# Kernel tuning notes

Measured on AMD Instinct MI355X. Metric: run time of the kernel, lower is better.

Reference implementation:

```python
import jax, jax.numpy as jnp
import numpy as np

REG = 1e-6

def maxpool2(x):  # NCHW, kernel 2 stride 2
    return jax.lax.reduce_window(x, -jnp.inf, jax.lax.max, (1, 1, 2, 2), (1, 1, 2, 2), 'VALID')

def conv2d_same(x, w, b):  # NCHW / OIHW, stride 1, padding 1 (3x3)
    y = jax.lax.conv_general_dilated(x, w, (1, 1), ((1, 1), (1, 1)),
                                     dimension_numbers=('NCHW', 'OIHW', 'NCHW'))
    return y + b[None, :, None, None]

def batch_skew(a):  # [B,3] -> [B,3,3]
    z = jnp.zeros_like(a[:, 0])
    return jnp.stack([
        jnp.stack([z, -a[:, 2], a[:, 1]], -1),
        jnp.stack([a[:, 2], z, -a[:, 0]], -1),
        jnp.stack([-a[:, 1], a[:, 0], z], -1)], 1)

def batch_twist2mat(w):  # Rodrigues: so(3) -> SO(3)
    theta = jnp.maximum(jnp.linalg.norm(w, axis=1, keepdims=True), 1e-12)  # [B,1]
    A = batch_skew(w / theta)
    s = jnp.sin(theta)[:, :, None]
    c = (1.0 - jnp.cos(theta))[:, :, None]
    return jnp.eye(3, dtype=w.dtype) + s * A + c * (A @ A)

def setup_inputs() -> dict:
    key = jax.random.key(0)
    ks = jax.random.split(key, 24)
    B, C, H, W = 64, 8, 240, 320
    HW = H * W
    A = jax.random.normal(ks[0], (B, 6, 6), jnp.float32)
    JtJ = A @ jnp.swapaxes(A, 1, 2) + 6.0 * jnp.eye(6, dtype=jnp.float32)  # SPD Hessian
    inp = {
        'JtJ': JtJ,
        'Jt': jax.random.normal(ks[1], (B, 6, HW), jnp.float32),
        'weights': jax.random.uniform(ks[2], (B, 1, H, W), jnp.float32),
        'R': jax.random.normal(ks[3], (B, 1, H, W), jnp.float32),
        'pose_R': jax.random.normal(ks[4], (B, 3, 3), jnp.float32),
        'pose_t': jax.random.normal(ks[5], (B, 3, 1), jnp.float32),
        'invD0': jax.random.uniform(ks[6], (B, 1, H, W), jnp.float32),
        'invD1': jax.random.uniform(ks[7], (B, 1, H, W), jnp.float32),
        'x0': jax.random.normal(ks[8], (B, C, H, W), jnp.float32),
        'x1': jax.random.normal(ks[9], (B, C, H, W), jnp.float32),
        'K': jax.random.normal(ks[10], (B, 3, 3), jnp.float32),
        # DampingNet parameters
        'consts': jax.random.normal(ks[11], (6, 6), jnp.float32),
        'conv1_w': jax.random.normal(ks[12], (8, 1, 3, 3), jnp.float32) * 0.2,
        'conv1_b': jnp.zeros((8,), jnp.float32),
        'conv2_w': jax.random.normal(ks[13], (16, 8, 3, 3), jnp.float32) * 0.1,
        'conv2_b': jnp.zeros((16,), jnp.float32),
        'fc1_w': jax.random.normal(ks[14], (64, 19200), jnp.float32) * 0.01,
        'fc1_b': jnp.zeros((64,), jnp.float32),
        'fc2_w': jax.random.normal(ks[15], (6, 64), jnp.float32) * 0.1,
        'fc2_b': jnp.zeros((6,), jnp.float32),
    }
    return inp

def dampingnet(R, consts, c1w, c1b, c2w, c2b, f1w, f1b, f2w, f2b):
    B = R.shape[0]
    h = maxpool2(R)
    h = jax.nn.relu(conv2d_same(h, c1w, c1b))
    h = maxpool2(h)
    h = jax.nn.relu(conv2d_same(h, c2w, c2b))
    h = maxpool2(h)
    h = h.reshape(B, -1)  # [B, 19200], NCHW flatten matches torch
    h = jax.nn.relu(h @ f1w.T + f1b)
    lambdas_w = jax.nn.softmax(h @ f2w.T + f2b, axis=-1)  # [B,6]
    wc = lambdas_w @ consts  # [B,6]
    min_, max_ = -6.0, -5.0
    return 10.0 ** (min_ + jax.nn.sigmoid(wc) * (max_ - min_))  # [B,6]

def reference(JtJ, Jt, weights, R, pose_R, pose_t, invD0, invD1, x0, x1, K,
              consts, conv1_w, conv1_b, conv2_w, conv2_b, fc1_w, fc1_b, fc2_w, fc2_b):
    B = JtJ.shape[0]
    wR = (weights * R).reshape(B, -1, 1)            # [B,HW,1]
    JtR = Jt @ wR                                   # [B,6,1]
    lam = dampingnet(R, consts, conv1_w, conv1_b, conv2_w, conv2_b,
                     fc1_w, fc1_b, fc2_w, fc2_b)    # [B,6]
    trace = jnp.trace(JtJ, axis1=1, axis2=2)        # [B]
    diag_add = lam + 1e-6 * trace[:, None]          # [B,6]
    eye6 = jnp.eye(6, dtype=JtJ.dtype)
    Hessian = JtJ + diag_add[:, :, None] * eye6     # diag_mask*lambda + epsilon
    # inverse_update_pose: regularized batched 6x6 inverse
    Hinv = jnp.linalg.inv(Hessian + REG * eye6)
    xi = Hinv @ JtR                                 # [B,6,1]
    d_R = batch_twist2mat(-xi[:, :3, 0])            # [B,3,3]
    d_t = -(d_R @ xi[:, 3:])                        # [B,3,1]
    R_new = pose_R @ d_R
    t_new = pose_R @ d_t + pose_t
    return jnp.concatenate([R_new, t_new], axis=2)  # [B,3,4] pose (R|t)
```

## Files before the change

kernel.cpp:

```cpp
#include <hip/hip_runtime.h>
#include <math.h>

#define BATCH 64
#define WW 320
#define HWTOT 76800
#define HW4 19200
#define NJTRB 512
#define JSL4 2400
#define NCONV1 1280
#define KS 64
#define NSLICE 300

typedef _Float16 half2_t __attribute__((ext_vector_type(2)));
union U32H2 { unsigned int u; half2_t h; };
__device__ __forceinline__ unsigned int pack_h2(float a, float b) {
  U32H2 x; x.h = half2_t{(_Float16)a, (_Float16)b}; return x.u;
}
__device__ __forceinline__ half2_t u_as_h2(unsigned int u) { U32H2 x; x.u = u; return x.h; }

#if defined(__has_builtin)
#if __has_builtin(__builtin_amdgcn_fdot2)
#define HAVE_FDOT2 1
#endif
#endif

__device__ __forceinline__ float dot2acc(unsigned int a, unsigned int b, float c) {
#ifdef HAVE_FDOT2
  return __builtin_amdgcn_fdot2(u_as_h2(a), u_as_h2(b), c, false);
#else
  half2_t ah = u_as_h2(a), bh = u_as_h2(b);
  return c + (float)ah.x * (float)bh.x + (float)ah.y * (float)bh.y;
#endif
}

__global__ __launch_bounds__(256) void k_front(
    const float* __restrict__ Jt, const float* __restrict__ wgt,
    const float* __restrict__ Rin, const float* __restrict__ c1w,
    const float* __restrict__ c1b, const float* __restrict__ c2w,
    float* __restrict__ part, unsigned int* __restrict__ h1u,
    unsigned int* __restrict__ wpk) {
  __shared__ float smem[34 * 37 + 96];
  int tid = threadIdx.x;
  if (blockIdx.x < NJTRB) {
    int b = blockIdx.x >> 3, s = blockIdx.x & 7;
    const float4* w4 = (const float4*)(wgt + (size_t)b * HWTOT);
    const float4* r4 = (const float4*)(Rin + (size_t)b * HWTOT);
    const float4* j4 = (const float4*)(Jt + (size_t)b * 6 * HWTOT);
    int base = s * JSL4;
    float acc[6] = {0.f, 0.f, 0.f, 0.f, 0.f, 0.f};
#pragma unroll 3
    for (int k = 0; k < 9; ++k) {
      int t = base + k * 256 + tid;
      float4 wv = w4[t], rv = r4[t];
      float4 p;
      p.x = wv.x * rv.x; p.y = wv.y * rv.y; p.z = wv.z * rv.z; p.w = wv.w * rv.w;
#pragma unroll
      for (int i = 0; i < 6; ++i) {
        float4 jv = j4[i * HW4 + t];
        acc[i] += jv.x * p.x + jv.y * p.y + jv.z * p.z + jv.w * p.w;
      }
    }
    if (tid < 96) {
      int t = base + 2304 + tid;
      float4 wv = w4[t], rv = r4[t];
      float4 p;
      p.x = wv.x * rv.x; p.y = wv.y * rv.y; p.z = wv.z * rv.z; p.w = wv.w * rv.w;
#pragma unroll
      for (int i = 0; i < 6; ++i) {
        float4 jv = j4[i * HW4 + t];
        acc[i] += jv.x * p.x + jv.y * p.y + jv.z * p.z + jv.w * p.w;
      }
    }
#pragma unroll
    for (int i = 0; i < 6; ++i) {
      float v = acc[i];
      for (int off = 32; off; off >>= 1) v += __shfl_down(v, off, 64);
      acc[i] = v;
    }
    float* sred = smem;
    int lane = tid & 63, wid = tid >> 6;
    if (lane == 0) {
#pragma unroll
      for (int i = 0; i < 6; ++i) sred[wid * 6 + i] = acc[i];
    }
    __syncthreads();
    if (tid < 6) {
      part[blockIdx.x * 6 + tid] =
          sred[0 + tid] + sred[6 + tid] + sred[12 + tid] + sred[18 + tid];
    }
    return;
  }
  int cb = blockIdx.x - NJTRB;
  int b = cb / 20, rem = cb % 20;
  int by = rem / 5, bx = rem % 5;
  if (cb == 0) {
    for (int i = tid; i < 576; i += 256) {
      int ocg = i / 288, tap = (i % 288) / 32, o = (i % 32) / 4, icp = i % 4;
      int oc = ocg * 8 + o;
      float lo = c2w[oc * 72 + (2 * icp) * 9 + tap];
      float hi = c2w[oc * 72 + (2 * icp + 1) * 9 + tap];
      wpk[i] = pack_h2(lo, hi);
    }
  }
  float (*sA)[37] = (float(*)[37])smem;
  float* sW = smem + 34 * 37;
  float* sB = sW + 72;
  if (tid < 72) sW[tid] = c1w[(tid & 7) * 9 + (tid >> 3)];
  if (tid < 8) sB[tid] = c1b[tid];
  int iy0 = 32 * by - 1;
  const float* src = Rin + (size_t)b * HWTOT;
  for (int idx = tid; idx < 34 * 18; idx += 256) {
    int pr = idx / 18, c4 = idx % 18;
    int py = iy0 + pr;
    int gx = 64 * bx - 4 + 4 * c4;
    float cell0 = 0.f, cell1 = 0.f;
    if (py >= 0 && py < 120 && gx >= 0 && gx < 320) {
      const float4* row0 = (const float4*)(src + (size_t)(2 * py) * WW + gx);
      const float4* row1 = (const float4*)(src + (size_t)(2 * py + 1) * WW + gx);
      float4 v0 = row0[0], v1 = row1[0];
      cell0 = fmaxf(fmaxf(v0.x, v0.y), fmaxf(v1.x, v1.y));
      cell1 = fmaxf(fmaxf(v0.z, v0.w), fmaxf(v1.z, v1.w));
    }
    sA[pr][2 * c4] = cell0;
    sA[pr][2 * c4 + 1] = cell1;
  }
  __syncthreads();
  int ly = tid / 16, lx = tid % 16;
  int y = 16 * by + ly, x = 16 * bx + lx;
  float win[16];
#pragma unroll
  for (int r = 0; r < 4; ++r)
#pragma unroll
    for (int c = 0; c < 4; ++c) win[r * 4 + c] = sA[2 * ly + r][2 * lx + c + 1];
  float acc[8][4];
#pragma unroll
  for (int oc = 0; oc < 8; ++oc)
#pragma unroll
    for (int p = 0; p < 4; ++p) acc[oc][p] = 0.f;
#pragma unroll
  for (int tap = 0; tap < 9; ++tap) {
    int ky = tap / 3, kx = tap % 3;
#pragma unroll
    for (int oc = 0; oc < 8; ++oc) {
      float wv = sW[tap * 8 + oc];
#pragma unroll
      for (int py = 0; py < 2; ++py)
#pragma unroll
        for (int px = 0; px < 2; ++px)
          acc[oc][py * 2 + px] += wv * win[(py + ky) * 4 + (px + kx)];
    }
  }
  if (y < 60) {
    float v[8];
#pragma unroll
    for (int oc = 0; oc < 8; ++oc)
      v[oc] = fmaxf(fmaxf(fmaxf(acc[oc][0], acc[oc][1]), fmaxf(acc[oc][2], acc[oc][3])) + sB[oc], 0.f);
    uint4 st;
    st.x = pack_h2(v[0], v[1]);
    st.y = pack_h2(v[2], v[3]);
    st.z = pack_h2(v[4], v[5]);
    st.w = pack_h2(v[6], v[7]);
    *(uint4*)(h1u + (((size_t)b * 60 + y) * 80 + x) * 4) = st;
  }
}

__global__ __launch_bounds__(256) void k_conv2(
    const unsigned int* __restrict__ h1u, const unsigned int* __restrict__ wpk,
    const float* __restrict__ c2b, float* __restrict__ h2) {
  __shared__ __align__(16) uint4 sA[34][36];
  int b = blockIdx.z >> 1, ocg = blockIdx.z & 1;
  int ty0 = blockIdx.y * 16, tx0 = blockIdx.x * 16;
  int tid = threadIdx.x;
  int iy0 = ty0 * 2 - 1, ix0 = tx0 * 2 - 1;
  const unsigned int* src = h1u + (size_t)b * 60 * 80 * 4;
  for (int idx = tid; idx < 34 * 34; idx += 256) {
    int r = idx / 34, c = idx % 34;
    int gy = iy0 + r, gx = ix0 + c;
    uint4 v = make_uint4(0u, 0u, 0u, 0u);
    if (gy >= 0 && gy < 60 && gx >= 0 && gx < 80)
      v = *(const uint4*)(src + ((size_t)gy * 80 + gx) * 4);
    sA[r][c] = v;
  }
  __syncthreads();
  int ly = tid / 16, lx = tid % 16;
  uint4 win[16];
#pragma unroll
  for (int r = 0; r < 4; ++r)
#pragma unroll
    for (int c = 0; c < 4; ++c) win[r * 4 + c] = sA[2 * ly + r][2 * lx + c];
  float acc[8][4];
#pragma unroll
  for (int o = 0; o < 8; ++o)
#pragma unroll
    for (int p = 0; p < 4; ++p) acc[o][p] = 0.f;
  const uint4* wq = (const uint4*)wpk + ocg * 72;
#pragma unroll
  for (int tap = 0; tap < 9; ++tap) {
    int ky = tap / 3, kx = tap % 3;
#pragma unroll
    for (int o = 0; o < 8; ++o) {
      uint4 wv = wq[tap * 8 + o];
#pragma unroll
      for (int py = 0; py < 2; ++py)
#pragma unroll
        for (int px = 0; px < 2; ++px) {
          uint4 wn = win[(py + ky) * 4 + (px + kx)];
          float a = acc[o][py * 2 + px];
          a = dot2acc(wn.x, wv.x, a);
          a = dot2acc(wn.y, wv.y, a);
          a = dot2acc(wn.z, wv.z, a);
          a = dot2acc(wn.w, wv.w, a);
          acc[o][py * 2 + px] = a;
        }
    }
  }
  int y = ty0 + ly, x = tx0 + lx;
  if (y < 30 && x < 40) {
#pragma unroll
    for (int o = 0; o < 8; ++o) {
      int oc = ocg * 8 + o;
      float m = fmaxf(fmaxf(acc[o][0], acc[o][1]), fmaxf(acc[o][2], acc[o][3])) + c2b[oc];
      h2[(((size_t)b * 16 + oc) * 30 + y) * 40 + x] = fmaxf(m, 0.f);
    }
  }
}

__global__ __launch_bounds__(256) void k_fc1_part(
    const float* __restrict__ h2, const float* __restrict__ f1w,
    float* __restrict__ fcpart) {
  __shared__ __align__(16) float sH[KS * 68];
  __shared__ __align__(16) float sWt[KS * 68];
  int sl = blockIdx.x, k0 = sl * KS;
  int tid = threadIdx.x;
  for (int idx = tid; idx < 64 * KS; idx += 256) {
    int b = idx >> 6, kk = idx & 63;
    sH[kk * 68 + b] = h2[(size_t)b * 19200 + k0 + kk];
    sWt[kk * 68 + b] = f1w[(size_t)b * 19200 + k0 + kk];
  }
  __syncthreads();
  int bq = tid & 15, jq = tid >> 4;
  int b0 = bq * 4, j0 = jq * 4;
  float acc[4][4];
#pragma unroll
  for (int i = 0; i < 4; ++i)
#pragma unroll
    for (int j = 0; j < 4; ++j) acc[i][j] = 0.f;
  for (int kk = 0; kk < KS; ++kk) {
    float4 hv = *(const float4*)&sH[kk * 68 + b0];
    float4 wv = *(const float4*)&sWt[kk * 68 + j0];
    float hb[4] = {hv.x, hv.y, hv.z, hv.w};
    float wb[4] = {wv.x, wv.y, wv.z, wv.w};
#pragma unroll
    for (int i = 0; i < 4; ++i)
#pragma unroll
      for (int j = 0; j < 4; ++j) acc[i][j] += hb[i] * wb[j];
  }
#pragma unroll
  for (int i = 0; i < 4; ++i)
#pragma unroll
    for (int j = 0; j < 4; ++j)
      fcpart[(size_t)(b0 + i) * 19200 + sl * 64 + (j0 + j)] = acc[i][j];
}

__global__ __launch_bounds__(256) void k_final(
    const float* __restrict__ fcpart, const float* __restrict__ f1b,
    const float* __restrict__ f2w, const float* __restrict__ f2b,
    const float* __restrict__ consts, const float* __restrict__ part,
    const float* __restrict__ JtJ, const float* __restrict__ poseR,
    const float* __restrict__ poseT, float* __restrict__ out) {
  __shared__ __align__(16) float sred[16 * 64];
  __shared__ float fc1v[64];
  __shared__ float sf2w[384];
  __shared__ float sf2b[8];
  __shared__ float sconst[36];
  __shared__ float lg[6];
  __shared__ float lamv[6];
  __shared__ float jtrv[6];
  int b = blockIdx.x, tid = threadIdx.x;
  for (int i = tid; i < 384; i += 256) sf2w[i] = f2w[i];
  if (tid < 6) sf2b[tid] = f2b[tid];
  if (tid < 36) sconst[tid] = consts[tid];
  {
    const float4* fp4 = (const float4*)(fcpart + (size_t)b * 19200);
    int sg = tid >> 4, j4 = tid & 15;
    float4 a = make_float4(0.f, 0.f, 0.f, 0.f);
    for (int s = sg; s < NSLICE; s += 16) {
      float4 v = fp4[s * 16 + j4];
      a.x += v.x; a.y += v.y; a.z += v.z; a.w += v.w;
    }
    ((float4*)sred)[sg * 16 + j4] = a;
  }
  if (tid >= 64 && tid < 70) {
    int i = tid - 64;
    float v = 0.f;
    for (int s = 0; s < 8; ++s) v += part[(b * 8 + s) * 6 + i];
    jtrv[i] = v;
  }
  __syncthreads();
  if (tid < 64) {
    float v = 0.f;
#pragma unroll
    for (int sg = 0; sg < 16; ++sg) v += sred[sg * 64 + tid];
    fc1v[tid] = fmaxf(v + f1b[tid], 0.f);
  }
  __syncthreads();
  if (tid < 6) {
    float v = sf2b[tid];
#pragma unroll
    for (int k = 0; k < 64; ++k) v += fc1v[k] * sf2w[tid * 64 + k];
    lg[tid] = v;
  }
  __syncthreads();
  if (tid < 6) {
    float m = lg[0];
#pragma unroll
    for (int i = 1; i < 6; ++i) m = fmaxf(m, lg[i]);
    float e[6], ssum = 0.f;
#pragma unroll
    for (int i = 0; i < 6; ++i) { e[i] = expf(lg[i] - m); ssum += e[i]; }
    float inv = 1.f / ssum;
    float wc = 0.f;
#pragma unroll
    for (int i = 0; i < 6; ++i) wc += (e[i] * inv) * sconst[i * 6 + tid];
    float sg = 1.f / (1.f + expf(-wc));
    lamv[tid] = expf((-6.f + sg) * 2.302585092994046f);
  }
  __syncthreads();
  if (tid == 0) {
    float Hm[6][6];
    const float* srcH = JtJ + b * 36;
    float tr = 0.f;
#pragma unroll
    for (int i = 0; i < 6; ++i) {
#pragma unroll
      for (int jj = 0; jj < 6; ++jj) Hm[i][jj] = srcH[i * 6 + jj];
      tr += srcH[i * 6 + i];
    }
    float rhs[6];
#pragma unroll
    for (int i = 0; i < 6; ++i) {
      rhs[i] = jtrv[i];
      Hm[i][i] += lamv[i] + 1e-6f * tr + 1e-6f;
    }
    float L[6][6];
#pragma unroll
    for (int i = 0; i < 6; ++i) {
#pragma unroll
      for (int jj = 0; jj < 6; ++jj) {
        if (jj > i) continue;
        float s = Hm[i][jj];
#pragma unroll
        for (int k = 0; k < 6; ++k)
          if (k < jj) s -= L[i][k] * L[jj][k];
        if (i == jj) L[i][jj] = sqrtf(fmaxf(s, 1e-30f));
        else L[i][jj] = s / L[jj][jj];
      }
    }
    float yv[6];
#pragma unroll
    for (int i = 0; i < 6; ++i) {
      float s = rhs[i];
#pragma unroll
      for (int k = 0; k < 6; ++k)
        if (k < i) s -= L[i][k] * yv[k];
      yv[i] = s / L[i][i];
    }
    float xi[6];
#pragma unroll
    for (int ii = 5; ii >= 0; --ii) {
      float s = yv[ii];
#pragma unroll
      for (int k = 0; k < 6; ++k)
        if (k > ii) s -= L[k][ii] * xi[k];
      xi[ii] = s / L[ii][ii];
    }
    float wx = -xi[0], wy = -xi[1], wz = -xi[2];
    float th = fmaxf(sqrtf(wx * wx + wy * wy + wz * wz), 1e-12f);
    float ux = wx / th, uy = wy / th, uz = wz / th;
    float s = sinf(th), c1 = 1.f - cosf(th);
    float Rd[3][3];
    Rd[0][0] = 1.f + c1 * (ux * ux - 1.f);
    Rd[0][1] = -s * uz + c1 * (ux * uy);
    Rd[0][2] = s * uy + c1 * (ux * uz);
    Rd[1][0] = s * uz + c1 * (uy * ux);
    Rd[1][1] = 1.f + c1 * (uy * uy - 1.f);
    Rd[1][2] = -s * ux + c1 * (uy * uz);
    Rd[2][0] = -s * uy + c1 * (uz * ux);
    Rd[2][1] = s * ux + c1 * (uz * uy);
    Rd[2][2] = 1.f + c1 * (uz * uz - 1.f);
    float dt[3];
#pragma unroll
    for (int r = 0; r < 3; ++r)
      dt[r] = -(Rd[r][0] * xi[3] + Rd[r][1] * xi[4] + Rd[r][2] * xi[5]);
    const float* pR = poseR + b * 9;
    const float* pt = poseT + b * 3;
#pragma unroll
    for (int r = 0; r < 3; ++r) {
#pragma unroll
      for (int cc = 0; cc < 3; ++cc) {
        out[b * 12 + r * 4 + cc] =
            pR[r * 3 + 0] * Rd[0][cc] + pR[r * 3 + 1] * Rd[1][cc] + pR[r * 3 + 2] * Rd[2][cc];
      }
      out[b * 12 + r * 4 + 3] =
          pR[r * 3 + 0] * dt[0] + pR[r * 3 + 1] * dt[1] + pR[r * 3 + 2] * dt[2] + pt[r];
    }
  }
}

extern "C" void kernel_launch(void* const* d_in, const int* in_sizes, int n_in,
                              void* d_out, int out_size, void* d_ws, size_t ws_size,
                              hipStream_t stream) {
  const float* JtJ = (const float*)d_in[0];
  const float* Jt = (const float*)d_in[1];
  const float* wts = (const float*)d_in[2];
  const float* Rin = (const float*)d_in[3];
  const float* poseR = (const float*)d_in[4];
  const float* poseT = (const float*)d_in[5];
  const float* consts = (const float*)d_in[11];
  const float* c1w = (const float*)d_in[12];
  const float* c1b = (const float*)d_in[13];
  const float* c2w = (const float*)d_in[14];
  const float* c2b = (const float*)d_in[15];
  const float* f1w = (const float*)d_in[16];
  const float* f1b = (const float*)d_in[17];
  const float* f2w = (const float*)d_in[18];
  const float* f2b = (const float*)d_in[19];
  float* ws = (float*)d_ws;
  float* part = ws;
  unsigned int* h1u = (unsigned int*)(ws + 3072);
  float* h2 = ws + 3072 + 1228800;
  float* fcpart = h2 + 1228800;
  unsigned int* wpk = (unsigned int*)(fcpart + 1228800);
  float* out = (float*)d_out;

  k_front<<<dim3(NJTRB + NCONV1), dim3(256), 0, stream>>>(Jt, wts, Rin, c1w, c1b, c2w,
                                                          part, h1u, wpk);
  k_conv2<<<dim3(3, 2, BATCH * 2), dim3(256), 0, stream>>>(h1u, wpk, c2b, h2);
  k_fc1_part<<<dim3(NSLICE), dim3(256), 0, stream>>>(h2, f1w, fcpart);
  k_final<<<dim3(64), dim3(256), 0, stream>>>(fcpart, f1b, f2w, f2b, consts, part,
                                              JtJ, poseR, poseT, out);
}
```

Before: 65.14 us.

## Fuse conv1 and conv2 into front kernel with shared-memory halo tiles

Merges the conv1 (maxpool+conv+pool) and conv2 stages into one block that computes a haloed conv1 tile in shared memory, then runs conv2 on it. This drops the h1 round-trip through global memory and one kernel launch, and packs the conv2 weights per block instead of through a global workspace. In exchange, each block recomputes halo conv1 outputs, and two output-channel groups recompute the same conv1 tile. The fdot2 builtin path is also removed in favour of scalar half-to-float math, which may make the conv2 inner loop slower.

```diff
diff --git a/kernel.cpp b/kernel.cpp
--- a/kernel.cpp
+++ b/kernel.cpp
@@ -7,7 +7,7 @@
 #define HW4 19200
 #define NJTRB 512
 #define JSL4 2400
-#define NCONV1 1280
+#define NCONVB 768
 #define KS 64
 #define NSLICE 300
 
@@ -18,28 +18,27 @@
 }
 __device__ __forceinline__ half2_t u_as_h2(unsigned int u) { U32H2 x; x.u = u; return x.h; }
 
-#if defined(__has_builtin)
-#if __has_builtin(__builtin_amdgcn_fdot2)
-#define HAVE_FDOT2 1
-#endif
-#endif
-
 __device__ __forceinline__ float dot2acc(unsigned int a, unsigned int b, float c) {
-#ifdef HAVE_FDOT2
-  return __builtin_amdgcn_fdot2(u_as_h2(a), u_as_h2(b), c, false);
-#else
   half2_t ah = u_as_h2(a), bh = u_as_h2(b);
   return c + (float)ah.x * (float)bh.x + (float)ah.y * (float)bh.y;
-#endif
-}
+}
+
+#define SR_F 0
+#define SR_LD 71
+#define SH1_U4 (70 * 71)
+#define SH1_OFF_F 4972
+#define SW2_OFF_F (SH1_OFF_F + 34 * 35 * 4)
+#define SW1_OFF_F (SW2_OFF_F + 288)
+#define SB1_OFF_F (SW1_OFF_F + 72)
+#define SMEM_FLOATS (SB1_OFF_F + 8)
 
 __global__ __launch_bounds__(256) void k_front(
     const float* __restrict__ Jt, const float* __restrict__ wgt,
     const float* __restrict__ Rin, const float* __restrict__ c1w,
     const float* __restrict__ c1b, const float* __restrict__ c2w,
-    float* __restrict__ part, unsigned int* __restrict__ h1u,
-    unsigned int* __restrict__ wpk) {
-  __shared__ float smem[34 * 37 + 96];
+    const float* __restrict__ c2b, float* __restrict__ part,
+    float* __restrict__ h2) {
+  __shared__ __align__(16) float smem[SMEM_FLOATS];
   int tid = threadIdx.x;
   if (blockIdx.x < NJTRB) {
     int b = blockIdx.x >> 3, s = blockIdx.x & 7;
@@ -91,95 +90,81 @@
     return;
   }
   int cb = blockIdx.x - NJTRB;
-  int b = cb / 20, rem = cb % 20;
-  int by = rem / 5, bx = rem % 5;
-  if (cb == 0) {
-    for (int i = tid; i < 576; i += 256) {
-      int ocg = i / 288, tap = (i % 288) / 32, o = (i % 32) / 4, icp = i % 4;
-      int oc = ocg * 8 + o;
+  int b = cb / 12, q = cb % 12;
+  int tx = q % 3, ty = (q / 3) & 1, ocg = q / 6;
+  int ty0 = 16 * ty, tx0 = 16 * tx;
+  float* sR = smem + SR_F;
+  uint4* sH1 = (uint4*)(smem + SH1_OFF_F);
+  unsigned int* sW2 = (unsigned int*)(smem + SW2_OFF_F);
+  float* sW1 = smem + SW1_OFF_F;
+  float* sB1 = smem + SB1_OFF_F;
+  if (tid < 72) sW1[tid] = c1w[(tid & 7) * 9 + (tid >> 3)];
+  if (tid < 8) sB1[tid] = c1b[tid];
+  if (tid < 72) {
+    int tap = tid / 8, o = tid % 8;
+    int oc = ocg * 8 + o;
+#pragma unroll
+    for (int icp = 0; icp < 4; ++icp) {
       float lo = c2w[oc * 72 + (2 * icp) * 9 + tap];
       float hi = c2w[oc * 72 + (2 * icp + 1) * 9 + tap];
-      wpk[i] = pack_h2(lo, hi);
-    }
-  }
-  float (*sA)[37] = (float(*)[37])smem;
-  float* sW = smem + 34 * 37;
-  float* sB = sW + 72;
-  if (tid < 72) sW[tid] = c1w[(tid & 7) * 9 + (tid >> 3)];
-  if (tid < 8) sB[tid] = c1b[tid];
-  int iy0 = 32 * by - 1;
+      sW2[(tap * 8 + o) * 4 + icp] = pack_h2(lo, hi);
+    }
+  }
+  int pr0 = 64 * ty - 3, pc0 = 64 * tx - 3;
   const float* src = Rin + (size_t)b * HWTOT;
-  for (int idx = tid; idx < 34 * 18; idx += 256) {
-    int pr = idx / 18, c4 = idx % 18;
-    int py = iy0 + pr;
-    int gx = 64 * bx - 4 + 4 * c4;
-    float cell0 = 0.f, cell1 = 0.f;
-    if (py >= 0 && py < 120 && gx >= 0 && gx < 320) {
-      const float4* row0 = (const float4*)(src + (size_t)(2 * py) * WW + gx);
-      const float4* row1 = (const float4*)(src + (size_t)(2 * py + 1) * WW + gx);
-      float4 v0 = row0[0], v1 = row1[0];
-      cell0 = fmaxf(fmaxf(v0.x, v0.y), fmaxf(v1.x, v1.y));
-      cell1 = fmaxf(fmaxf(v0.z, v0.w), fmaxf(v1.z, v1.w));
-    }
-    sA[pr][2 * c4] = cell0;
-    sA[pr][2 * c4 + 1] = cell1;
-  }
-  __syncthreads();
-  int ly = tid / 16, lx = tid % 16;
-  int y = 16 * by + ly, x = 16 * bx + lx;
-  float win[16];
-#pragma unroll
-  for (int r = 0; r < 4; ++r)
-#pragma unroll
-    for (int c = 0; c < 4; ++c) win[r * 4 + c] = sA[2 * ly + r][2 * lx + c + 1];
-  float acc[8][4];
-#pragma unroll
-  for (int oc = 0; oc < 8; ++oc)
-#pragma unroll
-    for (int p = 0; p < 4; ++p) acc[oc][p] = 0.f;
-#pragma unroll
-  for (int tap = 0; tap < 9; ++tap) {
-    int ky = tap / 3, kx = tap % 3;
-#pragma unroll
-    for (int oc = 0; oc < 8; ++oc) {
-      float wv = sW[tap * 8 + oc];
-#pragma unroll
-      for (int py = 0; py < 2; ++py)
-#pragma unroll
-        for (int px = 0; px < 2; ++px)
-          acc[oc][py * 2 + px] += wv * win[(py + ky) * 4 + (px + kx)];
-    }
-  }
-  if (y < 60) {
-    float v[8];
-#pragma unroll
-    for (int oc = 0; oc < 8; ++oc)
-      v[oc] = fmaxf(fmaxf(fmaxf(acc[oc][0], acc[oc][1]), fmaxf(acc[oc][2], acc[oc][3])) + sB[oc], 0.f);
+  for (int idx = tid; idx < 70 * 70; idx += 256) {
+    int r = idx / 70, c = idx % 70;
+    int py = pr0 + r, px = pc0 + c;
+    float v = 0.f;
+    if (py >= 0 && py < 120 && px >= 0 && px < 160) {
+      const float2* r0 = (const float2*)(src + (size_t)(2 * py) * WW);
+      const float2* r1 = (const float2*)(src + (size_t)(2 * py + 1) * WW);
+      float2 a = r0[px], bb = r1[px];
+      v = fmaxf(fmaxf(a.x, a.y), fmaxf(bb.x, bb.y));
+    }
+    sR[r * SR_LD + c] = v;
+  }
+  __syncthreads();
+  for (int idx = tid; idx < 34 * 34; idx += 256) {
+    int r = idx / 34, c = idx % 34;
+    int hr = 32 * ty - 1 + r, hc = 32 * tx - 1 + c;
+    float v[8] = {0.f, 0.f, 0.f, 0.f, 0.f, 0.f, 0.f, 0.f};
+    if (hr >= 0 && hr < 60 && hc >= 0 && hc < 80) {
+      float wnd[16];
+#pragma unroll
+      for (int i = 0; i < 4; ++i)
+#pragma unroll
+        for (int j = 0; j < 4; ++j) wnd[i * 4 + j] = sR[(2 * r + i) * SR_LD + (2 * c + j)];
+      float pac[8][4];
+#pragma unroll
+      for (int o = 0; o < 8; ++o)
+#pragma unroll
+        for (int p = 0; p < 4; ++p) pac[o][p] = 0.f;
+#pragma unroll
+      for (int tap = 0; tap < 9; ++tap) {
+        int ky = tap / 3, kx = tap % 3;
+#pragma unroll
+        for (int o = 0; o < 8; ++o) {
+          float w = sW1[tap * 8 + o];
+#pragma unroll
+          for (int py = 0; py < 2; ++py)
+#pragma unroll
+            for (int px = 0; px < 2; ++px)
+              pac[o][py * 2 + px] += w * wnd[(py + ky) * 4 + (px + kx)];
+        }
+      }
+#pragma unroll
+      for (int o = 0; o < 8; ++o) {
+        float m = fmaxf(fmaxf(pac[o][0], pac[o][1]), fmaxf(pac[o][2], pac[o][3])) + sB1[o];
+        v[o] = fmaxf(m, 0.f);
+      }
+    }
     uint4 st;
     st.x = pack_h2(v[0], v[1]);
     st.y = pack_h2(v[2], v[3]);
     st.z = pack_h2(v[4], v[5]);
     st.w = pack_h2(v[6], v[7]);
-    *(uint4*)(h1u + (((size_t)b * 60 + y) * 80 + x) * 4) = st;
-  }
-}
-
-__global__ __launch_bounds__(256) void k_conv2(
-    const unsigned int* __restrict__ h1u, const unsigned int* __restrict__ wpk,
-    const float* __restrict__ c2b, float* __restrict__ h2) {
-  __shared__ __align__(16) uint4 sA[34][36];
-  int b = blockIdx.z >> 1, ocg = blockIdx.z & 1;
-  int ty0 = blockIdx.y * 16, tx0 = blockIdx.x * 16;
-  int tid = threadIdx.x;
-  int iy0 = ty0 * 2 - 1, ix0 = tx0 * 2 - 1;
-  const unsigned int* src = h1u + (size_t)b * 60 * 80 * 4;
-  for (int idx = tid; idx < 34 * 34; idx += 256) {
-    int r = idx / 34, c = idx % 34;
-    int gy = iy0 + r, gx = ix0 + c;
-    uint4 v = make_uint4(0u, 0u, 0u, 0u);
-    if (gy >= 0 && gy < 60 && gx >= 0 && gx < 80)
-      v = *(const uint4*)(src + ((size_t)gy * 80 + gx) * 4);
-    sA[r][c] = v;
+    sH1[r * 35 + c] = st;
   }
   __syncthreads();
   int ly = tid / 16, lx = tid % 16;
@@ -187,13 +172,13 @@
 #pragma unroll
   for (int r = 0; r < 4; ++r)
 #pragma unroll
-    for (int c = 0; c < 4; ++c) win[r * 4 + c] = sA[2 * ly + r][2 * lx + c];
+    for (int c = 0; c < 4; ++c) win[r * 4 + c] = sH1[(2 * ly + r) * 35 + (2 * lx + c)];
   float acc[8][4];
 #pragma unroll
   for (int o = 0; o < 8; ++o)
 #pragma unroll
     for (int p = 0; p < 4; ++p) acc[o][p] = 0.f;
-  const uint4* wq = (const uint4*)wpk + ocg * 72;
+  const uint4* wq = (const uint4*)sW2;
 #pragma unroll
   for (int tap = 0; tap < 9; ++tap) {
     int ky = tap / 3, kx = tap % 3;
@@ -427,15 +412,12 @@
   const float* f2b = (const float*)d_in[19];
   float* ws = (float*)d_ws;
   float* part = ws;
-  unsigned int* h1u = (unsigned int*)(ws + 3072);
-  float* h2 = ws + 3072 + 1228800;
+  float* h2 = part + 3072;
   float* fcpart = h2 + 1228800;
-  unsigned int* wpk = (unsigned int*)(fcpart + 1228800);
   float* out = (float*)d_out;
 
-  k_front<<<dim3(NJTRB + NCONV1), dim3(256), 0, stream>>>(Jt, wts, Rin, c1w, c1b, c2w,
-                                                          part, h1u, wpk);
-  k_conv2<<<dim3(3, 2, BATCH * 2), dim3(256), 0, stream>>>(h1u, wpk, c2b, h2);
+  k_front<<<dim3(NJTRB + NCONVB), dim3(256), 0, stream>>>(Jt, wts, Rin, c1w, c1b,
+                                                          c2w, c2b, part, h2);
   k_fc1_part<<<dim3(NSLICE), dim3(256), 0, stream>>>(h2, f1w, fcpart);
   k_final<<<dim3(64), dim3(256), 0, stream>>>(fcpart, f1b, f2w, f2b, consts, part,
                                               JtJ, poseR, poseT, out);
```

New measurement: 76.98 us. 1.18x slower.

## Split JtR reduction across conv1 and conv2 kernels to overlap work

Applied to the files above, without the earlier changes.

The weighted Jt·R reduction is split into two halves, one fused into the conv1 kernel and one into the conv2 kernel, with partial sums combined in the final kernel. This balances the bandwidth-heavy reduction against the small conv2 grid to fill the GPU better. The packed fp16 dot2 builtin path is also removed, so conv2 always uses scalar converts and multiplies, which may add ALU cost.

```diff
diff --git a/kernel.cpp b/kernel.cpp
--- a/kernel.cpp
+++ b/kernel.cpp
@@ -7,7 +7,6 @@
 #define HW4 19200
 #define NJTRB 512
 #define JSL4 2400
-#define NCONV1 1280
 #define KS 64
 #define NSLICE 300
 
@@ -18,22 +17,60 @@
 }
 __device__ __forceinline__ half2_t u_as_h2(unsigned int u) { U32H2 x; x.u = u; return x.h; }
 
-#if defined(__has_builtin)
-#if __has_builtin(__builtin_amdgcn_fdot2)
-#define HAVE_FDOT2 1
-#endif
-#endif
-
 __device__ __forceinline__ float dot2acc(unsigned int a, unsigned int b, float c) {
-#ifdef HAVE_FDOT2
-  return __builtin_amdgcn_fdot2(u_as_h2(a), u_as_h2(b), c, false);
-#else
   half2_t ah = u_as_h2(a), bh = u_as_h2(b);
   return c + (float)ah.x * (float)bh.x + (float)ah.y * (float)bh.y;
-#endif
-}
-
-__global__ __launch_bounds__(256) void k_front(
+}
+
+__device__ __forceinline__ void jtr_half(
+    const float* __restrict__ Jt, const float* __restrict__ wgt,
+    const float* __restrict__ Rin, float* __restrict__ part,
+    int b, int slot, int base, float* sred) {
+  int tid = threadIdx.x;
+  const float4* w4 = (const float4*)(wgt + (size_t)b * HWTOT);
+  const float4* r4 = (const float4*)(Rin + (size_t)b * HWTOT);
+  const float4* j4 = (const float4*)(Jt + (size_t)b * 6 * HWTOT);
+  float acc[6] = {0.f, 0.f, 0.f, 0.f, 0.f, 0.f};
+#pragma unroll 2
+  for (int k = 0; k < 4; ++k) {
+    int t = base + k * 256 + tid;
+    float4 wv = w4[t], rv = r4[t];
+    float4 p;
+    p.x = wv.x * rv.x; p.y = wv.y * rv.y; p.z = wv.z * rv.z; p.w = wv.w * rv.w;
+#pragma unroll
+    for (int i = 0; i < 6; ++i) {
+      float4 jv = j4[i * HW4 + t];
+      acc[i] += jv.x * p.x + jv.y * p.y + jv.z * p.z + jv.w * p.w;
+    }
+  }
+  if (tid < 176) {
+    int t = base + 1024 + tid;
+    float4 wv = w4[t], rv = r4[t];
+    float4 p;
+    p.x = wv.x * rv.x; p.y = wv.y * rv.y; p.z = wv.z * rv.z; p.w = wv.w * rv.w;
+#pragma unroll
+    for (int i = 0; i < 6; ++i) {
+      float4 jv = j4[i * HW4 + t];
+      acc[i] += jv.x * p.x + jv.y * p.y + jv.z * p.z + jv.w * p.w;
+    }
+  }
+#pragma unroll
+  for (int i = 0; i < 6; ++i) {
+    float v = acc[i];
+    for (int off = 32; off; off >>= 1) v += __shfl_down(v, off, 64);
+    acc[i] = v;
+  }
+  int lane = tid & 63, wid = tid >> 6;
+  if (lane == 0) {
+#pragma unroll
+    for (int i = 0; i < 6; ++i) sred[wid * 6 + i] = acc[i];
+  }
+  __syncthreads();
+  if (tid < 6)
+    part[slot * 6 + tid] = sred[tid] + sred[6 + tid] + sred[12 + tid] + sred[18 + tid];
+}
+
+__global__ __launch_bounds__(256) void k_front1(
     const float* __restrict__ Jt, const float* __restrict__ wgt,
     const float* __restrict__ Rin, const float* __restrict__ c1w,
     const float* __restrict__ c1b, const float* __restrict__ c2w,
@@ -43,51 +80,7 @@
   int tid = threadIdx.x;
   if (blockIdx.x < NJTRB) {
     int b = blockIdx.x >> 3, s = blockIdx.x & 7;
-    const float4* w4 = (const float4*)(wgt + (size_t)b * HWTOT);
-    const float4* r4 = (const float4*)(Rin + (size_t)b * HWTOT);
-    const float4* j4 = (const float4*)(Jt + (size_t)b * 6 * HWTOT);
-    int base = s * JSL4;
-    float acc[6] = {0.f, 0.f, 0.f, 0.f, 0.f, 0.f};
-#pragma unroll 3
-    for (int k = 0; k < 9; ++k) {
-      int t = base + k * 256 + tid;
-      float4 wv = w4[t], rv = r4[t];
-      float4 p;
-      p.x = wv.x * rv.x; p.y = wv.y * rv.y; p.z = wv.z * rv.z; p.w = wv.w * rv.w;
-#pragma unroll
-      for (int i = 0; i < 6; ++i) {
-        float4 jv = j4[i * HW4 + t];
-        acc[i] += jv.x * p.x + jv.y * p.y + jv.z * p.z + jv.w * p.w;
-      }
-    }
-    if (tid < 96) {
-      int t = base + 2304 + tid;
-      float4 wv = w4[t], rv = r4[t];
-      float4 p;
-      p.x = wv.x * rv.x; p.y = wv.y * rv.y; p.z = wv.z * rv.z; p.w = wv.w * rv.w;
-#pragma unroll
-      for (int i = 0; i < 6; ++i) {
-        float4 jv = j4[i * HW4 + t];
-        acc[i] += jv.x * p.x + jv.y * p.y + jv.z * p.z + jv.w * p.w;
-      }
-    }
-#pragma unroll
-    for (int i = 0; i < 6; ++i) {
-      float v = acc[i];
-      for (int off = 32; off; off >>= 1) v += __shfl_down(v, off, 64);
-      acc[i] = v;
-    }
-    float* sred = smem;
-    int lane = tid & 63, wid = tid >> 6;
-    if (lane == 0) {
-#pragma unroll
-      for (int i = 0; i < 6; ++i) sred[wid * 6 + i] = acc[i];
-    }
-    __syncthreads();
-    if (tid < 6) {
-      part[blockIdx.x * 6 + tid] =
-          sred[0 + tid] + sred[6 + tid] + sred[12 + tid] + sred[18 + tid];
-    }
+    jtr_half(Jt, wgt, Rin, part, b, blockIdx.x, s * JSL4, smem);
     return;
   }
   int cb = blockIdx.x - NJTRB;
@@ -164,13 +157,22 @@
   }
 }
 
-__global__ __launch_bounds__(256) void k_conv2(
-    const unsigned int* __restrict__ h1u, const unsigned int* __restrict__ wpk,
-    const float* __restrict__ c2b, float* __restrict__ h2) {
+__global__ __launch_bounds__(256) void k_front2(
+    const float* __restrict__ Jt, const float* __restrict__ wgt,
+    const float* __restrict__ Rin, const unsigned int* __restrict__ h1u,
+    const unsigned int* __restrict__ wpk, const float* __restrict__ c2b,
+    float* __restrict__ part, float* __restrict__ h2) {
   __shared__ __align__(16) uint4 sA[34][36];
-  int b = blockIdx.z >> 1, ocg = blockIdx.z & 1;
-  int ty0 = blockIdx.y * 16, tx0 = blockIdx.x * 16;
   int tid = threadIdx.x;
+  if (blockIdx.x < NJTRB) {
+    int b = blockIdx.x >> 3, s = blockIdx.x & 7;
+    jtr_half(Jt, wgt, Rin, part, b, NJTRB + blockIdx.x, s * JSL4 + 1200, (float*)sA);
+    return;
+  }
+  int cb = blockIdx.x - NJTRB;
+  int b = cb / 12, r12 = cb % 12;
+  int gx0 = r12 % 3, gy0 = (r12 / 3) % 2, ocg = r12 / 6;
+  int ty0 = gy0 * 16, tx0 = gx0 * 16;
   int iy0 = ty0 * 2 - 1, ix0 = tx0 * 2 - 1;
   const unsigned int* src = h1u + (size_t)b * 60 * 80 * 4;
   for (int idx = tid; idx < 34 * 34; idx += 256) {
@@ -293,7 +295,8 @@
   if (tid >= 64 && tid < 70) {
     int i = tid - 64;
     float v = 0.f;
-    for (int s = 0; s < 8; ++s) v += part[(b * 8 + s) * 6 + i];
+    for (int s = 0; s < 8; ++s)
+      v += part[(b * 8 + s) * 6 + i] + part[(NJTRB + b * 8 + s) * 6 + i];
     jtrv[i] = v;
   }
   __syncthreads();
@@ -427,15 +430,16 @@
   const float* f2b = (const float*)d_in[19];
   float* ws = (float*)d_ws;
   float* part = ws;
-  unsigned int* h1u = (unsigned int*)(ws + 3072);
-  float* h2 = ws + 3072 + 1228800;
+  unsigned int* h1u = (unsigned int*)(ws + 6144);
+  float* h2 = ws + 6144 + 1228800;
   float* fcpart = h2 + 1228800;
   unsigned int* wpk = (unsigned int*)(fcpart + 1228800);
   float* out = (float*)d_out;
 
-  k_front<<<dim3(NJTRB + NCONV1), dim3(256), 0, stream>>>(Jt, wts, Rin, c1w, c1b, c2w,
-                                                          part, h1u, wpk);
-  k_conv2<<<dim3(3, 2, BATCH * 2), dim3(256), 0, stream>>>(h1u, wpk, c2b, h2);
+  k_front1<<<dim3(NJTRB + 1280), dim3(256), 0, stream>>>(Jt, wts, Rin, c1w, c1b, c2w,
+                                                         part, h1u, wpk);
+  k_front2<<<dim3(NJTRB + 768), dim3(256), 0, stream>>>(Jt, wts, Rin, h1u, wpk, c2b,
+                                                        part, h2);
   k_fc1_part<<<dim3(NSLICE), dim3(256), 0, stream>>>(h2, f1w, fcpart);
   k_final<<<dim3(64), dim3(256), 0, stream>>>(fcpart, f1b, f2w, f2b, consts, part,
                                               JtJ, poseR, poseT, out);
```

Result: slower. 68.23 us (+4.7%).
